# Kernel optimization log

Hardware: AMD Instinct MI355X
Metric: run time of the kernel (lower is better)

## Reference

```python
import jax, jax.numpy as jnp
import numpy as np

N, L, D_MODEL, N_HEADS = 2, 2048, 512, 8

def setup_inputs() -> dict:
    key = jax.random.key(0)
    x = jax.random.normal(key, (N, L, D_MODEL), dtype=jnp.float32)
    return {"input_data": x}

def reference(input_data):
    n, l, _ = input_data.shape
    h = N_HEADS
    d = D_MODEL // h  # head dim
    # Q = K = V = reshaped input (the Linear projections are unused in the original forward)
    q = input_data.reshape(n, l, h, d)
    k = q
    v = q
    scale = 1.0 / jnp.sqrt(jnp.float32(d))
    # scores: [n, h, l, s]
    scores = jnp.einsum('nlhd,nshd->nhls', q, k)
    attn_weights = jax.nn.softmax(scale * scores, axis=-1)
    # updated values: [n, l, h, d]
    updated_v = jnp.einsum('nhls,nshd->nlhd', attn_weights, v)
    out = updated_v.reshape(n, l, h * d)
    # attn returned as mean over heads: permute nhls -> nlhs, mean over h -> [n, l, s]
    attn = jnp.transpose(attn_weights, (0, 2, 1, 3)).mean(axis=-2)
    return (out, attn)
```

## Files before the change

kernel.cpp:

```cpp
#include <hip/hip_runtime.h>

#define NBATCH 2
#define SEQ    2048
#define DMODEL 512
#define NH     8
#define HDIM   64
#define SCALE  0.125f

#define K2 0.1803368801111204f

#if __has_builtin(__builtin_amdgcn_exp2f)
#define EXP2(x) __builtin_amdgcn_exp2f(x)
#else
#define EXP2(x) __expf((x) * 0.6931471805599453f)
#endif

typedef __attribute__((ext_vector_type(8)))  short bf16x8;
typedef __attribute__((ext_vector_type(4)))  float f32x4;
typedef __attribute__((ext_vector_type(16))) float f32x16;

__device__ __forceinline__ unsigned short f2bf(float f) {
    union { float f; unsigned u; } v; v.f = f;
    unsigned r = v.u + 0x7FFFu + ((v.u >> 16) & 1u);
    return (unsigned short)(r >> 16);
}

__device__ __forceinline__ void pack4(unsigned short* dst, float4 v) {
    unsigned long long pk = (unsigned long long)f2bf(v.x)
        | ((unsigned long long)f2bf(v.y) << 16)
        | ((unsigned long long)f2bf(v.z) << 32)
        | ((unsigned long long)f2bf(v.w) << 48);
    __builtin_memcpy(dst, &pk, 8);
}

__device__ __forceinline__ bf16x8 pack8(float4 a, float4 b) {
    bf16x8 r;
    r[0]=(short)f2bf(a.x); r[1]=(short)f2bf(a.y); r[2]=(short)f2bf(a.z); r[3]=(short)f2bf(a.w);
    r[4]=(short)f2bf(b.x); r[5]=(short)f2bf(b.y); r[6]=(short)f2bf(b.z); r[7]=(short)f2bf(b.w);
    return r;
}

__device__ __forceinline__ unsigned cvt_pk_bf16(float s0, float s1) {
    unsigned d;
    asm("v_cvt_pk_bf16_f32 %0, %1, %2" : "=v"(d) : "v"(s0), "v"(s1));
    return d;
}

__device__ __forceinline__ void gld_lds16(const unsigned short* g, unsigned short* l) {
    __builtin_amdgcn_global_load_lds(
        (const __attribute__((address_space(1))) unsigned int*)(const void*)g,
        (__attribute__((address_space(3))) unsigned int*)(void*)l, 16, 0, 0);
}

__global__ __launch_bounds__(256) void prep_kernel(const float* __restrict__ x,
                                                   unsigned short* __restrict__ xb,
                                                   unsigned short* __restrict__ xt) {
    __shared__ unsigned short Tb[64][72];
    const int bid = blockIdx.x;
    const int n = bid >> 8, h = (bid >> 5) & 7, st = bid & 31;
    const int s0 = st * 64;
    const int t = threadIdx.x;
    {
        const int s = t >> 2, d0 = (t & 3) * 16;
        const float* xp = x + ((size_t)(n*SEQ + s0 + s))*DMODEL + h*HDIM + d0;
        #pragma unroll
        for (int i = 0; i < 4; ++i) pack4(&Tb[s][d0 + 4*i], *(const float4*)(xp + 4*i));
    }
    __syncthreads();
    {
        const int s = t >> 2, d0 = (t & 3) * 16;
        unsigned short* bp = xb + ((size_t)(n*SEQ + s0 + s))*DMODEL + h*HDIM + d0;
        *(bf16x8*)bp       = *(const bf16x8*)&Tb[s][d0];
        *(bf16x8*)(bp + 8) = *(const bf16x8*)&Tb[s][d0 + 8];
    }
    {
        const int d = t >> 2, c0 = (t & 3) * 16;
        bf16x8 v0, v1;
        #pragma unroll
        for (int j = 0; j < 8; ++j) {
            v0[j] = (short)Tb[c0 + j][d];
            v1[j] = (short)Tb[c0 + 8 + j][d];
        }
        unsigned short* tp = xt + ((size_t)((n*NH + h)*HDIM + d))*SEQ + s0 + c0;
        *(bf16x8*)tp       = v0;
        *(bf16x8*)(tp + 8) = v1;
    }
}

__global__ __launch_bounds__(256, 4) void out_kernel5(const unsigned short* __restrict__ xb,
                                                      const unsigned short* __restrict__ xt,
                                                      float* __restrict__ out,
                                                      float* __restrict__ rho,
                                                      float* __restrict__ part,
                                                      int split) {
    __shared__ unsigned short Kb[2][64*64];
    __shared__ unsigned short Vt[2][64*64];

    const int i   = blockIdx.x;
    const int cps = gridDim.x >> 3;
    const int bid = (i & 7) * cps + (i >> 3);
    int n, h, lt, ss;
    if (split) { n = bid >> 9; h = (bid >> 6) & 7; lt = (bid >> 1) & 31; ss = bid & 1; }
    else       { n = bid >> 8; h = (bid >> 5) & 7; lt = bid & 31;        ss = 0;       }
    const int l0 = lt * 64;
    const int sbase = ss << 10;
    const int nch = split ? 16 : 32;

    const int tid = threadIdx.x;
    const int wv = tid >> 6, lane = tid & 63;
    const int lrow = lane & 31;
    const int hi = lane >> 5;
    const int qh = wv & 1, sh = wv >> 1;

    const unsigned short* qg = xb + ((size_t)(n*SEQ + l0 + qh*32 + lrow))*DMODEL + h*HDIM;
    bf16x8 qf[4];
    #pragma unroll
    for (int kst = 0; kst < 4; ++kst)
        qf[kst] = *(const bf16x8*)(qg + kst*16 + hi*8);

    const int srow8  = wv*8 + (lane >> 3);
    const int schunk = lane & 7;
    const unsigned short* kbase = xb + (size_t)(n*SEQ)*DMODEL + h*HDIM;
    const unsigned short* vbase = xt + ((size_t)(n*NH + h)*HDIM)*SEQ;

    auto stage = [&](int buf, int s0) {
        #pragma unroll
        for (int it = 0; it < 2; ++it) {
            const int row = it*32 + srow8;
            const int gc  = schunk ^ (row & 7);
            gld_lds16(kbase + (size_t)(s0 + row)*DMODEL + gc*8,
                      &Kb[buf][it*2048 + wv*512]);
        }
        #pragma unroll
        for (int it = 0; it < 2; ++it) {
            const int d  = it*32 + srow8;
            const int gc = schunk ^ (d & 7);
            gld_lds16(vbase + (size_t)d*SEQ + s0 + gc*8,
                      &Vt[buf][it*2048 + wv*512]);
        }
    };

    f32x16 ovA = {0.f}, ovB = {0.f};
    #pragma unroll
    for (int r = 0; r < 16; ++r) { ovA[r] = 0.f; ovB[r] = 0.f; }
    float rs = 0.f;

    stage(0, sbase);
    __syncthreads();
    int cur = 0;

    for (int c = 0; c < nch; ++c) {
        if (c < nch - 1) stage(cur ^ 1, sbase + (c + 1) * 64);

        f32x16 acc;
        #pragma unroll
        for (int r = 0; r < 16; ++r) acc[r] = 0.f;
        #pragma unroll
        for (int kst = 0; kst < 4; ++kst) {
            const int g = ((kst*2 + hi) ^ (lrow & 7)) << 3;
            const bf16x8 kf = *(const bf16x8*)&Kb[cur][(sh*32 + lrow)*64 + g];
            acc = __builtin_amdgcn_mfma_f32_32x32x16_bf16(kf, qf[kst], acc, 0, 0, 0);
        }
        #pragma unroll
        for (int r = 0; r < 16; ++r) {
            acc[r] = EXP2(acc[r] * K2);
            rs += acc[r];
        }
        #pragma unroll
        for (int p = 0; p < 2; ++p) {
            const unsigned g0 = cvt_pk_bf16(acc[8*p+0], acc[8*p+1]);
            const unsigned g1 = cvt_pk_bf16(acc[8*p+2], acc[8*p+3]);
            const unsigned g2 = cvt_pk_bf16(acc[8*p+4], acc[8*p+5]);
            const unsigned g3 = cvt_pk_bf16(acc[8*p+6], acc[8*p+7]);
            const unsigned b0 = hi ? g0 : g2;
            const unsigned b1 = hi ? g1 : g3;
            const unsigned r0 = (unsigned)__shfl_xor((int)b0, 32);
            const unsigned r1 = (unsigned)__shfl_xor((int)b1, 32);
            union { unsigned u[4]; bf16x8 h8; } pf;
            pf.u[0] = hi ? r0 : g0;
            pf.u[1] = hi ? r1 : g1;
            pf.u[2] = hi ? g2 : r0;
            pf.u[3] = hi ? g3 : r1;
            const int gv = ((sh*4 + p*2 + hi) ^ (lrow & 7)) << 3;
            const bf16x8 v0 = *(const bf16x8*)&Vt[cur][( 0 + lrow)*64 + gv];
            const bf16x8 v1 = *(const bf16x8*)&Vt[cur][(32 + lrow)*64 + gv];
            ovA = __builtin_amdgcn_mfma_f32_32x32x16_bf16(v0, pf.h8, ovA, 0, 0, 0);
            ovB = __builtin_amdgcn_mfma_f32_32x32x16_bf16(v1, pf.h8, ovB, 0, 0, 0);
        }
        __syncthreads();
        cur ^= 1;
    }

    rs += __shfl_xor(rs, 32);
    float* red = (float*)&Vt[0][0];
    float* rsr = (float*)&Kb[0][0];
    if (sh == 1) {
        #pragma unroll
        for (int g = 0; g < 4; ++g) {
            float4 a = { ovA[4*g+0], ovA[4*g+1], ovA[4*g+2], ovA[4*g+3] };
            float4 b = { ovB[4*g+0], ovB[4*g+1], ovB[4*g+2], ovB[4*g+3] };
            *(float4*)&red[qh*2048 + lrow*64 +  0 + g*8 + 4*hi] = a;
            *(float4*)&red[qh*2048 + lrow*64 + 32 + g*8 + 4*hi] = b;
        }
        if (hi == 0) rsr[qh*32 + lrow] = rs;
    }
    __syncthreads();
    if (sh == 0) {
        const float rs_tot = rs + rsr[qh*32 + lrow];
        #pragma unroll
        for (int g = 0; g < 4; ++g) {
            float4 a = *(const float4*)&red[qh*2048 + lrow*64 +  0 + g*8 + 4*hi];
            float4 b = *(const float4*)&red[qh*2048 + lrow*64 + 32 + g*8 + 4*hi];
            ovA[4*g+0]+=a.x; ovA[4*g+1]+=a.y; ovA[4*g+2]+=a.z; ovA[4*g+3]+=a.w;
            ovB[4*g+0]+=b.x; ovB[4*g+1]+=b.y; ovB[4*g+2]+=b.z; ovB[4*g+3]+=b.w;
        }
        const int qloc = qh*32 + lrow;
        if (split) {
            float* pp = part + ((size_t)(((n*NH + h)*32 + lt)*2 + ss))*4160;
            #pragma unroll
            for (int g = 0; g < 4; ++g) {
                float4 a = { ovA[4*g+0], ovA[4*g+1], ovA[4*g+2], ovA[4*g+3] };
                float4 b = { ovB[4*g+0], ovB[4*g+1], ovB[4*g+2], ovB[4*g+3] };
                *(float4*)&pp[qloc*64 +  0 + g*8 + 4*hi] = a;
                *(float4*)&pp[qloc*64 + 32 + g*8 + 4*hi] = b;
            }
            if (hi == 0) pp[4096 + qloc] = rs_tot;
        } else {
            const float iv = 1.f / rs_tot;
            float* op = out + ((size_t)(n*SEQ + l0 + qloc))*DMODEL + h*HDIM;
            #pragma unroll
            for (int g = 0; g < 4; ++g) {
                float4 a = { ovA[4*g+0]*iv, ovA[4*g+1]*iv, ovA[4*g+2]*iv, ovA[4*g+3]*iv };
                float4 b = { ovB[4*g+0]*iv, ovB[4*g+1]*iv, ovB[4*g+2]*iv, ovB[4*g+3]*iv };
                *(float4*)&op[ 0 + g*8 + 4*hi] = a;
                *(float4*)&op[32 + g*8 + 4*hi] = b;
            }
            if (hi == 0) rho[(size_t)(n*NH + h)*SEQ + l0 + qloc] = rs_tot;
        }
    }
}

__global__ __launch_bounds__(256) void mean_kernel6(const unsigned short* __restrict__ xb,
                                                    const float* __restrict__ rho,
                                                    const float* __restrict__ part,
                                                    float* __restrict__ out,
                                                    float* __restrict__ attn) {
    __shared__ unsigned short Qb[2][64*64];
    __shared__ unsigned short Kb[2][64*64];
    __shared__ float invb[NH][64];

    const int i   = blockIdx.x;
    const int bid = (i & 7) * 256 + (i >> 3);
    const int n = bid >> 10, lt = (bid >> 5) & 31, st = bid & 31;
    const int l0 = lt * 64, s0 = st * 64;
    const int tid = threadIdx.x;
    const int wv = tid >> 6, lane = tid & 63;
    const int lr = lane & 15, lg = lane >> 4;

    const int srow8  = wv*8 + (lane >> 3);
    const int schunk = lane & 7;

    auto stage = [&](int buf, int h) {
        #pragma unroll
        for (int it = 0; it < 2; ++it) {
            const int row = it*32 + srow8;
            const int gc  = schunk ^ (row & 7);
            gld_lds16(xb + ((size_t)(n*SEQ + l0 + row))*DMODEL + h*HDIM + gc*8,
                      &Qb[buf][it*2048 + wv*512]);
        }
        #pragma unroll
        for (int it = 0; it < 2; ++it) {
            const int row = it*32 + srow8;
            const int gc  = schunk ^ (row & 7);
            gld_lds16(xb + ((size_t)(n*SEQ + s0 + row))*DMODEL + h*HDIM + gc*8,
                      &Kb[buf][it*2048 + wv*512]);
        }
    };

    stage(0, 0);

    if (part != nullptr && st < NH) {
        const int hC = st;
        const float* p0 = part + ((size_t)(((n*NH + hC)*32 + lt)*2))*4160;
        const float* p1 = p0 + 4160;
        const int q = tid >> 2, dg = (tid & 3) * 16;
        const float rsT = p0[4096 + q] + p1[4096 + q];
        const float iv = 1.f / rsT;
        float* op = out + ((size_t)(n*SEQ + l0 + q))*DMODEL + hC*HDIM + dg;
        #pragma unroll
        for (int k = 0; k < 4; ++k) {
            float4 a = *(const float4*)&p0[q*64 + dg + 4*k];
            float4 b = *(const float4*)&p1[q*64 + dg + 4*k];
            float4 o = { (a.x+b.x)*iv, (a.y+b.y)*iv, (a.z+b.z)*iv, (a.w+b.w)*iv };
            *(float4*)&op[4*k] = o;
        }
    }

    for (int j = tid; j < NH*64; j += 256) {
        const int hh = j >> 6, row = j & 63;
        float rv;
        if (part != nullptr) {
            const float* pb_ = part + ((size_t)(((n*NH + hh)*32 + lt)*2))*4160 + 4096;
            rv = pb_[row] + pb_[4160 + row];
        } else {
            rv = rho[(size_t)(n*NH + hh)*SEQ + l0 + row];
        }
        invb[hh][row] = 0.125f / rv;
    }

    float mean[4][4];
    #pragma unroll
    for (int ct = 0; ct < 4; ++ct)
        #pragma unroll
        for (int r = 0; r < 4; ++r) mean[ct][r] = 0.f;

    __syncthreads();
    int cur = 0;

    for (int h = 0; h < NH; ++h) {
        if (h < NH-1) stage(cur ^ 1, h + 1);

        const int qrow = wv*16 + lr;
        const int c0 = (lg ^ (lr & 7)) << 3;
        const bf16x8 a0 = *(const bf16x8*)&Qb[cur][qrow*64 + c0];
        const bf16x8 a1 = *(const bf16x8*)&Qb[cur][qrow*64 + (c0 ^ 32)];
        const float logiv = __log2f(invb[h][qrow]);
        #pragma unroll
        for (int ct = 0; ct < 4; ++ct) {
            const unsigned short* kr = &Kb[cur][(ct*16 + lr)*64];
            bf16x8 b0 = *(const bf16x8*)&kr[c0];
            bf16x8 b1 = *(const bf16x8*)&kr[c0 ^ 32];
            f32x4 acc = {0.f,0.f,0.f,0.f};
            acc = __builtin_amdgcn_mfma_f32_16x16x32_bf16(b0, a0, acc, 0,0,0);
            acc = __builtin_amdgcn_mfma_f32_16x16x32_bf16(b1, a1, acc, 0,0,0);
            #pragma unroll
            for (int r = 0; r < 4; ++r)
                mean[ct][r] += EXP2(fmaf(acc[r], K2, logiv));
        }
        __syncthreads();
        cur ^= 1;
    }

    const int arow = n*SEQ + l0 + wv*16 + lr;
    #pragma unroll
    for (int ct = 0; ct < 4; ++ct) {
        float4 v = { mean[ct][0], mean[ct][1], mean[ct][2], mean[ct][3] };
        *(float4*)&attn[(size_t)arow*SEQ + s0 + ct*16 + lg*4] = v;
    }
}

__global__ __launch_bounds__(256) void fb_out_kernel(const float* __restrict__ x,
                                                     float* __restrict__ out,
                                                     float* __restrict__ rho) {
    __shared__ unsigned short Kbuf[128][72];
    __shared__ unsigned short vT[64][136];
    __shared__ unsigned short pbuf[64][136];
    const int bid = blockIdx.x;
    const int n  = bid >> 8, h = (bid >> 5) & 7, lt = bid & 31;
    const int l0 = lt * 64;
    const int tid = threadIdx.x;
    const int wv  = tid >> 6, lane = tid & 63;
    const int lr  = lane & 15, lg = lane >> 4;
    const float* qp = x + ((size_t)(n*SEQ + l0 + wv*16 + lr))*DMODEL + h*HDIM + lg*8;
    const bf16x8 a0 = pack8(*(const float4*)qp,      *(const float4*)(qp+4));
    const bf16x8 a1 = pack8(*(const float4*)(qp+32), *(const float4*)(qp+36));
    f32x4 ov0 = {0.f,0.f,0.f,0.f}, ov1 = {0.f,0.f,0.f,0.f};
    f32x4 ov2 = {0.f,0.f,0.f,0.f}, ov3 = {0.f,0.f,0.f,0.f};
    float rs[4] = {0.f,0.f,0.f,0.f};
    for (int s0 = 0; s0 < SEQ; s0 += 128) {
        __syncthreads();
        {
            const int srow = tid >> 1, dbase = (tid & 1) * 32;
            const float* kp = x + ((size_t)(n*SEQ + s0 + srow))*DMODEL + h*HDIM + dbase;
            #pragma unroll
            for (int i = 0; i < 8; ++i) {
                float4 v = *(const float4*)(kp + 4*i);
                pack4(&Kbuf[srow][dbase + 4*i], v);
                const int d = dbase + 4*i;
                vT[d+0][srow] = f2bf(v.x); vT[d+1][srow] = f2bf(v.y);
                vT[d+2][srow] = f2bf(v.z); vT[d+3][srow] = f2bf(v.w);
            }
        }
        __syncthreads();
        #pragma unroll
        for (int ct = 0; ct < 8; ++ct) {
            const unsigned short* bp = &Kbuf[ct*16 + lr][lg*8];
            bf16x8 b0 = *(const bf16x8*)bp;
            bf16x8 b1 = *(const bf16x8*)(bp + 32);
            f32x4 acc = {0.f,0.f,0.f,0.f};
            acc = __builtin_amdgcn_mfma_f32_16x16x32_bf16(a0, b0, acc, 0,0,0);
            acc = __builtin_amdgcn_mfma_f32_16x16x32_bf16(a1, b1, acc, 0,0,0);
            #pragma unroll
            for (int r = 0; r < 4; ++r) {
                const float e = __expf(acc[r] * SCALE);
                rs[r] += e;
                pbuf[wv*16 + lg*4 + r][ct*16 + lr] = f2bf(e);
            }
        }
        __syncthreads();
        #pragma unroll
        for (int ks = 0; ks < 4; ++ks) {
            bf16x8 pa = *(const bf16x8*)&pbuf[wv*16 + lr][ks*32 + lg*8];
            bf16x8 v0 = *(const bf16x8*)&vT[ 0 + lr][ks*32 + lg*8];
            bf16x8 v1 = *(const bf16x8*)&vT[16 + lr][ks*32 + lg*8];
            bf16x8 v2 = *(const bf16x8*)&vT[32 + lr][ks*32 + lg*8];
            bf16x8 v3 = *(const bf16x8*)&vT[48 + lr][ks*32 + lg*8];
            ov0 = __builtin_amdgcn_mfma_f32_16x16x32_bf16(pa, v0, ov0, 0,0,0);
            ov1 = __builtin_amdgcn_mfma_f32_16x16x32_bf16(pa, v1, ov1, 0,0,0);
            ov2 = __builtin_amdgcn_mfma_f32_16x16x32_bf16(pa, v2, ov2, 0,0,0);
            ov3 = __builtin_amdgcn_mfma_f32_16x16x32_bf16(pa, v3, ov3, 0,0,0);
        }
    }
    #pragma unroll
    for (int r = 0; r < 4; ++r) {
        float s = rs[r];
        s += __shfl_xor(s, 1, 16); s += __shfl_xor(s, 2, 16);
        s += __shfl_xor(s, 4, 16); s += __shfl_xor(s, 8, 16);
        rs[r] = s;
    }
    const int row0 = l0 + wv*16 + lg*4;
    if (lr == 0) {
        #pragma unroll
        for (int r = 0; r < 4; ++r)
            rho[(size_t)(n*NH + h)*SEQ + row0 + r] = rs[r];
    }
    #pragma unroll
    for (int r = 0; r < 4; ++r) {
        const float iv = 1.f / rs[r];
        float* op = out + ((size_t)(n*SEQ + row0 + r))*DMODEL + h*HDIM + lr;
        op[0] = ov0[r]*iv; op[16] = ov1[r]*iv; op[32] = ov2[r]*iv; op[48] = ov3[r]*iv;
    }
}

__global__ __launch_bounds__(256) void fb_mean_kernel(const float* __restrict__ x,
                                                      const float* __restrict__ rho,
                                                      float* __restrict__ attn) {
    __shared__ unsigned short Qb[64][72];
    __shared__ unsigned short Kb[128][72];
    __shared__ float          invb[64];
    const int bid = blockIdx.x;
    const int n  = bid >> 9, lt = (bid >> 4) & 31, st = bid & 15;
    const int l0 = lt * 64, s0 = st * 128;
    const int tid = threadIdx.x;
    const int wv  = tid >> 6, lane = tid & 63;
    const int lr  = lane & 15, lg = lane >> 4;
    float mean[8][4];
    #pragma unroll
    for (int ct = 0; ct < 8; ++ct)
        #pragma unroll
        for (int r = 0; r < 4; ++r) mean[ct][r] = 0.f;
    for (int h = 0; h < NH; ++h) {
        __syncthreads();
        {
            const int qrow = tid >> 2, qd = (tid & 3) * 16;
            const float* qp = x + ((size_t)(n*SEQ + l0 + qrow))*DMODEL + h*HDIM + qd;
            #pragma unroll
            for (int i = 0; i < 4; ++i)
                pack4(&Qb[qrow][qd + 4*i], *(const float4*)(qp + 4*i));
        }
        {
            const int srow = tid >> 1, dbase = (tid & 1) * 32;
            const float* kp = x + ((size_t)(n*SEQ + s0 + srow))*DMODEL + h*HDIM + dbase;
            #pragma unroll
            for (int i = 0; i < 8; ++i)
                pack4(&Kb[srow][dbase + 4*i], *(const float4*)(kp + 4*i));
        }
        if (tid < 64)
            invb[tid] = 0.125f / rho[(size_t)(n*NH + h)*SEQ + l0 + tid];
        __syncthreads();
        const unsigned short* ap = &Qb[wv*16 + lr][lg*8];
        const bf16x8 a0 = *(const bf16x8*)ap;
        const bf16x8 a1 = *(const bf16x8*)(ap + 32);
        #pragma unroll
        for (int ct = 0; ct < 8; ++ct) {
            const unsigned short* bp = &Kb[ct*16 + lr][lg*8];
            bf16x8 b0 = *(const bf16x8*)bp;
            bf16x8 b1 = *(const bf16x8*)(bp + 32);
            f32x4 acc = {0.f,0.f,0.f,0.f};
            acc = __builtin_amdgcn_mfma_f32_16x16x32_bf16(a0, b0, acc, 0,0,0);
            acc = __builtin_amdgcn_mfma_f32_16x16x32_bf16(a1, b1, acc, 0,0,0);
            #pragma unroll
            for (int r = 0; r < 4; ++r)
                mean[ct][r] += __expf(acc[r] * SCALE) * invb[wv*16 + lg*4 + r];
        }
    }
    #pragma unroll
    for (int ct = 0; ct < 8; ++ct)
        #pragma unroll
        for (int r = 0; r < 4; ++r)
            attn[((size_t)(n*SEQ + l0 + wv*16 + lg*4 + r))*SEQ + s0 + ct*16 + lr]
                = mean[ct][r];
}

extern "C" void kernel_launch(void* const* d_in, const int* in_sizes, int n_in,
                              void* d_out, int out_size, void* d_ws, size_t ws_size,
                              hipStream_t stream) {
    (void)in_sizes; (void)n_in; (void)out_size;
    const float* x = (const float*)d_in[0];
    float* out  = (float*)d_out;
    float* attn = out + (size_t)NBATCH*SEQ*DMODEL;
    float* rho  = (float*)d_ws;

    const size_t XB_OFF   = 131072;
    const size_t XT_OFF   = XB_OFF + 4194304;
    const size_t NEED1    = XT_OFF + 4194304;
    const size_t PART_OFF = NEED1;
    const size_t NEED2    = PART_OFF + (size_t)1024*4160*4;

    if (ws_size >= NEED1) {
        unsigned short* xb = (unsigned short*)((char*)d_ws + XB_OFF);
        unsigned short* xt = (unsigned short*)((char*)d_ws + XT_OFF);
        prep_kernel <<<dim3(512),  dim3(256), 0, stream>>>(x, xb, xt);
        if (ws_size >= NEED2) {
            float* part = (float*)((char*)d_ws + PART_OFF);
            out_kernel5 <<<dim3(1024), dim3(256), 0, stream>>>(xb, xt, out, rho, part, 1);
            mean_kernel6<<<dim3(2048), dim3(256), 0, stream>>>(xb, rho, part, out, attn);
        } else {
            out_kernel5 <<<dim3(512),  dim3(256), 0, stream>>>(xb, xt, out, rho, nullptr, 0);
            mean_kernel6<<<dim3(2048), dim3(256), 0, stream>>>(xb, rho, nullptr, out, attn);
        }
    } else {
        fb_out_kernel <<<dim3(512),  dim3(256), 0, stream>>>(x, out, rho);
        fb_mean_kernel<<<dim3(1024), dim3(256), 0, stream>>>(x, rho, attn);
    }
}
```

Baseline: 75.92 us.

## Exploit score symmetry to compute only upper-triangular attn-mean tiles

Because Q equals K, the raw score matrix is symmetric, so the mean kernel now launches only the upper-triangular (lt<=st) tile pairs. Each block computes the exp of the scores once and accumulates two means: one normalized by the row sums and one by the column sums. The second is transposed through LDS and written to the mirrored tile. This roughly halves the MFMA and exp work and the Q/K staging traffic, at the cost of extra accumulators, an LDS transpose, a serial loop to decode the tile index, and a launch-bounds occupancy hint.

After: 147.7 us. 1.95x slower.

```diff
diff --git a/kernel.cpp b/kernel.cpp
--- a/kernel.cpp
+++ b/kernel.cpp
@@ -240,18 +240,24 @@
     }
 }
 
-__global__ __launch_bounds__(256) void mean_kernel6(const unsigned short* __restrict__ xb,
-                                                    const float* __restrict__ rho,
-                                                    const float* __restrict__ part,
-                                                    float* __restrict__ out,
-                                                    float* __restrict__ attn) {
+__global__ __launch_bounds__(256, 4) void mean_kernel7(const unsigned short* __restrict__ xb,
+                                                       const float* __restrict__ rho,
+                                                       const float* __restrict__ part,
+                                                       float* __restrict__ out,
+                                                       float* __restrict__ attn) {
     __shared__ unsigned short Qb[2][64*64];
     __shared__ unsigned short Kb[2][64*64];
-    __shared__ float invb[NH][64];
+    __shared__ float invbL[NH][64];
+    __shared__ float invbS[NH][64];
 
     const int i   = blockIdx.x;
-    const int bid = (i & 7) * 256 + (i >> 3);
-    const int n = bid >> 10, lt = (bid >> 5) & 31, st = bid & 31;
+    const int bid = (i & 7) * 132 + (i >> 3);
+    const int n = bid / 528;
+    const int t = bid - n * 528;
+    int lt = 0, rem = t;
+    while (rem >= 32 - lt) { rem -= 32 - lt; ++lt; }
+    const int st = lt + rem;
+    const int diag = (lt == st);
     const int l0 = lt * 64, s0 = st * 64;
     const int tid = threadIdx.x;
     const int wv = tid >> 6, lane = tid & 63;
@@ -279,14 +285,14 @@
 
     stage(0, 0);
 
-    if (part != nullptr && st < NH) {
-        const int hC = st;
-        const float* p0 = part + ((size_t)(((n*NH + hC)*32 + lt)*2))*4160;
+    if (part != nullptr && t < 256) {
+        const int hC = t & 7, ltC = t >> 3;
+        const float* p0 = part + ((size_t)(((n*NH + hC)*32 + ltC)*2))*4160;
         const float* p1 = p0 + 4160;
         const int q = tid >> 2, dg = (tid & 3) * 16;
         const float rsT = p0[4096 + q] + p1[4096 + q];
         const float iv = 1.f / rsT;
-        float* op = out + ((size_t)(n*SEQ + l0 + q))*DMODEL + hC*HDIM + dg;
+        float* op = out + ((size_t)(n*SEQ + ltC*64 + q))*DMODEL + hC*HDIM + dg;
         #pragma unroll
         for (int k = 0; k < 4; ++k) {
             float4 a = *(const float4*)&p0[q*64 + dg + 4*k];
@@ -298,33 +304,38 @@
 
     for (int j = tid; j < NH*64; j += 256) {
         const int hh = j >> 6, row = j & 63;
-        float rv;
+        float rvL, rvS;
         if (part != nullptr) {
-            const float* pb_ = part + ((size_t)(((n*NH + hh)*32 + lt)*2))*4160 + 4096;
-            rv = pb_[row] + pb_[4160 + row];
+            const float* pL = part + ((size_t)(((n*NH + hh)*32 + lt)*2))*4160 + 4096;
+            const float* pS = part + ((size_t)(((n*NH + hh)*32 + st)*2))*4160 + 4096;
+            rvL = pL[row] + pL[4160 + row];
+            rvS = pS[row] + pS[4160 + row];
         } else {
-            rv = rho[(size_t)(n*NH + hh)*SEQ + l0 + row];
-        }
-        invb[hh][row] = 0.125f / rv;
-    }
-
-    float mean[4][4];
+            rvL = rho[(size_t)(n*NH + hh)*SEQ + l0 + row];
+            rvS = rho[(size_t)(n*NH + hh)*SEQ + s0 + row];
+        }
+        invbL[hh][row] = 0.125f / rvL;
+        invbS[hh][row] = 0.125f / rvS;
+    }
+
+    float meanL[4][4], meanT[4][4];
     #pragma unroll
     for (int ct = 0; ct < 4; ++ct)
         #pragma unroll
-        for (int r = 0; r < 4; ++r) mean[ct][r] = 0.f;
+        for (int r = 0; r < 4; ++r) { meanL[ct][r] = 0.f; meanT[ct][r] = 0.f; }
 
     __syncthreads();
     int cur = 0;
 
+    const int qrow = wv*16 + lr;
+
     for (int h = 0; h < NH; ++h) {
         if (h < NH-1) stage(cur ^ 1, h + 1);
 
-        const int qrow = wv*16 + lr;
         const int c0 = (lg ^ (lr & 7)) << 3;
         const bf16x8 a0 = *(const bf16x8*)&Qb[cur][qrow*64 + c0];
         const bf16x8 a1 = *(const bf16x8*)&Qb[cur][qrow*64 + (c0 ^ 32)];
-        const float logiv = __log2f(invb[h][qrow]);
+        const float ivL = invbL[h][qrow];
         #pragma unroll
         for (int ct = 0; ct < 4; ++ct) {
             const unsigned short* kr = &Kb[cur][(ct*16 + lr)*64];
@@ -333,19 +344,48 @@
             f32x4 acc = {0.f,0.f,0.f,0.f};
             acc = __builtin_amdgcn_mfma_f32_16x16x32_bf16(b0, a0, acc, 0,0,0);
             acc = __builtin_amdgcn_mfma_f32_16x16x32_bf16(b1, a1, acc, 0,0,0);
-            #pragma unroll
-            for (int r = 0; r < 4; ++r)
-                mean[ct][r] += EXP2(fmaf(acc[r], K2, logiv));
+            const float4 ivS = *(const float4*)&invbS[h][ct*16 + lg*4];
+            const float e0 = EXP2(acc[0] * K2);
+            const float e1 = EXP2(acc[1] * K2);
+            const float e2 = EXP2(acc[2] * K2);
+            const float e3 = EXP2(acc[3] * K2);
+            meanL[ct][0] += e0 * ivL;  meanT[ct][0] += e0 * ivS.x;
+            meanL[ct][1] += e1 * ivL;  meanT[ct][1] += e1 * ivS.y;
+            meanL[ct][2] += e2 * ivL;  meanT[ct][2] += e2 * ivS.z;
+            meanL[ct][3] += e3 * ivL;  meanT[ct][3] += e3 * ivS.w;
         }
         __syncthreads();
         cur ^= 1;
     }
 
-    const int arow = n*SEQ + l0 + wv*16 + lr;
-    #pragma unroll
-    for (int ct = 0; ct < 4; ++ct) {
-        float4 v = { mean[ct][0], mean[ct][1], mean[ct][2], mean[ct][3] };
-        *(float4*)&attn[(size_t)arow*SEQ + s0 + ct*16 + lg*4] = v;
+    {
+        const size_t arow = (size_t)(n*SEQ + l0 + qrow);
+        #pragma unroll
+        for (int ct = 0; ct < 4; ++ct) {
+            float4 v = { meanL[ct][0], meanL[ct][1], meanL[ct][2], meanL[ct][3] };
+            *(float4*)&attn[arow*SEQ + s0 + ct*16 + lg*4] = v;
+        }
+    }
+
+    if (!diag) {
+        float* T = (float*)&Qb[0][0];
+        #pragma unroll
+        for (int ct = 0; ct < 4; ++ct) {
+            #pragma unroll
+            for (int r = 0; r < 4; ++r) {
+                const int s = ct*16 + lg*4 + r;
+                T[s*64 + ((((qrow >> 2) ^ (s & 15)) << 2) | (qrow & 3))] = meanT[ct][r];
+            }
+        }
+        __syncthreads();
+        const int srow = tid >> 2;
+        const size_t trow = (size_t)(n*SEQ + s0 + srow);
+        #pragma unroll
+        for (int j4 = 0; j4 < 4; ++j4) {
+            const int jg = (tid & 3) * 4 + j4;
+            float4 v = *(const float4*)&T[srow*64 + ((jg ^ (srow & 15)) << 2)];
+            *(float4*)&attn[trow*SEQ + l0 + (jg << 2)] = v;
+        }
     }
 }
 
@@ -514,10 +554,10 @@
         if (ws_size >= NEED2) {
             float* part = (float*)((char*)d_ws + PART_OFF);
             out_kernel5 <<<dim3(1024), dim3(256), 0, stream>>>(xb, xt, out, rho, part, 1);
-            mean_kernel6<<<dim3(2048), dim3(256), 0, stream>>>(xb, rho, part, out, attn);
+            mean_kernel7<<<dim3(1056), dim3(256), 0, stream>>>(xb, rho, part, out, attn);
         } else {
             out_kernel5 <<<dim3(512),  dim3(256), 0, stream>>>(xb, xt, out, rho, nullptr, 0);
-            mean_kernel6<<<dim3(2048), dim3(256), 0, stream>>>(xb, rho, nullptr, out, attn);
+            mean_kernel7<<<dim3(1056), dim3(256), 0, stream>>>(xb, rho, nullptr, out, attn);
         }
     } else {
         fb_out_kernel <<<dim3(512),  dim3(256), 0, stream>>>(x, out, rho);
```
